# Performance work log

Measured on AMD Instinct MI355X. Metric: run time of the kernel, lower is better.

Reference implementation:

```python
import jax, jax.numpy as jnp
import numpy as np

B, D, H, DH = 2048, 1024, 8, 64  # batch, query_dim, heads, dim_head
INNER = H * DH  # 512


def setup_inputs() -> dict:
    key = jax.random.key(0)
    k0, k1, k2, k3 = jax.random.split(key, 4)
    x = jax.random.normal(k0, (B, D), dtype=jnp.float32)
    Wq = jax.random.normal(k1, (D, INNER), dtype=jnp.float32) * 0.02
    Wkv = jax.random.normal(k2, (D, 2 * INNER), dtype=jnp.float32) * 0.02
    Wout = jax.random.normal(k3, (INNER, D), dtype=jnp.float32) * 0.02
    bout = jnp.zeros((D,), dtype=jnp.float32)
    return {"x": x, "Wq": Wq, "Wkv": Wkv, "Wout": Wout, "bout": bout}


def reference(x, Wq, Wkv, Wout, bout):
    # Faithful to the original: 2D x, attention over the flattened (B*H) axis.
    b = x.shape[0]
    scale = DH ** -0.5
    q = (x @ Wq).reshape(b * H, DH)            # (b h) d
    k, v = jnp.split(x @ Wkv, 2, axis=-1)      # each [b, inner]
    k = k.reshape(b * H, DH)
    v = v.reshape(b * H, DH)
    sim = (q @ k.T) * scale                    # [(b h), (b h)] -- 1 GB intermediate
    attn = jax.nn.softmax(sim, axis=-1)        # dropout_rate = 0 -> identity
    out = (attn @ v).reshape(b, INNER)         # b (h d)
    return out @ Wout + bout                   # project_out path
```

## Files before the change

### kernel.cpp

```cpp
#include <hip/hip_runtime.h>
#include <hip/hip_bf16.h>
#include <stdint.h>


typedef __bf16 bf16_t;
typedef __bf16 bf16x4 __attribute__((ext_vector_type(4)));
typedef __bf16 bf16x8 __attribute__((ext_vector_type(8)));
typedef float floatx4 __attribute__((ext_vector_type(4)));

__device__ __forceinline__ floatx4 mfma16(bf16x8 a, bf16x8 b, floatx4 c) {
    return __builtin_amdgcn_mfma_f32_16x16x32_bf16(a, b, c, 0, 0, 0);
}

__device__ __forceinline__ bf16x8 cvt8(float4 a, float4 b) {
    bf16x8 o;
    o[0] = (bf16_t)a.x; o[1] = (bf16_t)a.y; o[2] = (bf16_t)a.z; o[3] = (bf16_t)a.w;
    o[4] = (bf16_t)b.x; o[5] = (bf16_t)b.y; o[6] = (bf16_t)b.z; o[7] = (bf16_t)b.w;
    return o;
}

__device__ __forceinline__ void transpose_body(const float* __restrict__ in, int N,
                                               bf16_t* __restrict__ out, int ldo,
                                               int bx, int by, int tid, float (*tile)[33]) {
    int n0 = bx * 32, k0 = by * 32;
    int tx = tid & 31, ty = tid >> 5;
#pragma unroll
    for (int i = 0; i < 32; i += 8)
        tile[ty + i][tx] = in[(size_t)(k0 + ty + i) * N + (n0 + tx)];
    __syncthreads();
#pragma unroll
    for (int i = 0; i < 32; i += 8)
        out[(size_t)(n0 + ty + i) * ldo + (k0 + tx)] = (bf16_t)tile[tx][ty + i];
}

__global__ __launch_bounds__(256) void prep_all(const float* __restrict__ x,
                                                bf16_t* __restrict__ xb,
                                                const float* __restrict__ Wq,
                                                const float* __restrict__ Wkv,
                                                const float* __restrict__ Wout,
                                                bf16_t* __restrict__ WtQKV,
                                                bf16_t* __restrict__ WtOut) {
    __shared__ float tile[32][33];
    int b = blockIdx.x, tid = threadIdx.x;
    if (b < 1024) {
        int i = (b * 256 + tid) * 8;
        *(bf16x8*)(xb + i) = cvt8(*(const float4*)(x + i), *(const float4*)(x + i + 4));
    } else if (b < 1536) {
        b -= 1024;
        transpose_body(Wq, 512, WtQKV, 1024, b & 15, b >> 4, tid, tile);
    } else if (b < 2560) {
        b -= 1536;
        transpose_body(Wkv, 1024, WtQKV + 512 * 1024, 1024, b & 31, b >> 5, tid, tile);
    } else {
        b -= 2560;
        transpose_body(Wout, 1024, WtOut, 512, b & 31, b >> 5, tid, tile);
    }
}

template <int OF32, int MI>
__global__ __launch_bounds__(256) void gemm_bt(const bf16_t* __restrict__ A,
                                               const bf16_t* __restrict__ Bt,
                                               const float* __restrict__ bias,
                                               void* __restrict__ Cout,
                                               bf16_t* __restrict__ VtOut, int vt_col0,
                                               int K, int lda, int ldb, int ldc,
                                               float qscale, int qcols) {
    constexpr int MT = MI * 32;
    constexpr int PA = MT / 64;
    __shared__ bf16_t sA[MT * 64];
    __shared__ bf16_t sB[64 * 64];
    int tid = threadIdx.x;
    int wave = tid >> 6, lane = tid & 63;
    int lm = lane & 15, q = lane >> 4;
    int bm = blockIdx.x * MT, bn = blockIdx.y * 64;
    int wm = (wave >> 1) * (MT / 2), wn = (wave & 1) * 32;

    int c0 = (tid & 3) * 2, c1 = c0 + 1;
    int rA[PA], swA[PA];
    size_t srcA0[PA], srcA1[PA];
#pragma unroll
    for (int p = 0; p < PA; ++p) {
        rA[p] = p * 64 + (tid >> 2);
        swA[p] = rA[p] & 7;
        srcA0[p] = (size_t)(bm + rA[p]) * lda + ((c0 ^ swA[p]) << 3);
        srcA1[p] = (size_t)(bm + rA[p]) * lda + ((c1 ^ swA[p]) << 3);
    }
    int rB = tid >> 2, swB = rB & 7;
    size_t srcB0 = (size_t)(bn + rB) * ldb + ((c0 ^ swB) << 3);
    size_t srcB1 = (size_t)(bn + rB) * ldb + ((c1 ^ swB) << 3);

    floatx4 acc[MI][2];
#pragma unroll
    for (int i = 0; i < MI; ++i)
#pragma unroll
        for (int j = 0; j < 2; ++j) acc[i][j] = (floatx4){0.f, 0.f, 0.f, 0.f};

    bf16x8 pa0[PA], pa1[PA], pb0, pb1;
#pragma unroll
    for (int p = 0; p < PA; ++p) {
        pa0[p] = *(const bf16x8*)(A + srcA0[p]);
        pa1[p] = *(const bf16x8*)(A + srcA1[p]);
    }
    pb0 = *(const bf16x8*)(Bt + srcB0);
    pb1 = *(const bf16x8*)(Bt + srcB1);
#pragma unroll
    for (int p = 0; p < PA; ++p) {
        *(bf16x8*)&sA[p * 4096 + tid * 16] = pa0[p];
        *(bf16x8*)&sA[p * 4096 + tid * 16 + 8] = pa1[p];
    }
    *(bf16x8*)&sB[tid * 16] = pb0;
    *(bf16x8*)&sB[tid * 16 + 8] = pb1;
    __syncthreads();

    for (int k0 = 0; k0 < K; k0 += 64) {
        int kn = (k0 + 64 < K) ? k0 + 64 : 0;
#pragma unroll
        for (int p = 0; p < PA; ++p) {
            pa0[p] = *(const bf16x8*)(A + srcA0[p] + kn);
            pa1[p] = *(const bf16x8*)(A + srcA1[p] + kn);
        }
        pb0 = *(const bf16x8*)(Bt + srcB0 + kn);
        pb1 = *(const bf16x8*)(Bt + srcB1 + kn);

#pragma unroll
        for (int s = 0; s < 2; ++s) {
            int cs = s * 4 + q;
            bf16x8 af[MI], bfr[2];
#pragma unroll
            for (int i = 0; i < MI; ++i) {
                int row = wm + i * 16 + lm;
                af[i] = *(bf16x8*)&sA[row * 64 + ((cs ^ (lm & 7)) << 3)];
            }
#pragma unroll
            for (int j = 0; j < 2; ++j) {
                int row = wn + j * 16 + lm;
                bfr[j] = *(bf16x8*)&sB[row * 64 + ((cs ^ (lm & 7)) << 3)];
            }
#pragma unroll
            for (int i = 0; i < MI; ++i)
#pragma unroll
                for (int j = 0; j < 2; ++j)
                    acc[i][j] = mfma16(af[i], bfr[j], acc[i][j]);
        }

        __syncthreads();
#pragma unroll
        for (int p = 0; p < PA; ++p) {
            *(bf16x8*)&sA[p * 4096 + tid * 16] = pa0[p];
            *(bf16x8*)&sA[p * 4096 + tid * 16 + 8] = pa1[p];
        }
        *(bf16x8*)&sB[tid * 16] = pb0;
        *(bf16x8*)&sB[tid * 16 + 8] = pb1;
        __syncthreads();
    }

#pragma unroll
    for (int i = 0; i < MI; ++i)
#pragma unroll
        for (int j = 0; j < 2; ++j)
#pragma unroll
            for (int r = 0; r < 4; ++r) {
                int row = bm + wm + i * 16 + q * 4 + r;
                int col = bn + wn + j * 16 + lm;
                float v = acc[i][j][r];
                if (col < qcols) v *= qscale;
                if (bias) v += bias[col];
                if (col >= vt_col0) {
                    int cc = col - vt_col0;
                    VtOut[(size_t)(cc & 63) * 16384 + row * 8 + (cc >> 6)] = (bf16_t)v;
                } else {
                    size_t off = (size_t)row * ldc + col;
                    if (OF32) ((float*)Cout)[off] = v;
                    else      ((bf16_t*)Cout)[off] = (bf16_t)v;
                }
            }
}

__global__ __launch_bounds__(256, 2) void flash_attn(const bf16_t* __restrict__ QK,
                                                     const bf16_t* __restrict__ Vt,
                                                     bf16_t* __restrict__ O,
                                                     float* __restrict__ accP,
                                                     float* __restrict__ lP,
                                                     int kps, int nsplit) {
    __shared__ bf16_t sK[2][64 * 64];
    __shared__ bf16_t sVt[2][64 * 64];
    int tid = threadIdx.x;
    int wave = tid >> 6, lane = tid & 63;
    int lm = lane & 15, q = lane >> 4;
    int sp = blockIdx.y;
    int qrow0 = blockIdx.x * 256 + wave * 64;

    bf16x8 qf[4][2];
#pragma unroll
    for (int sub = 0; sub < 4; ++sub) {
        int qr = qrow0 + sub * 16 + lm;
        const bf16_t* qp = QK + (size_t)(qr >> 3) * 1024 + (qr & 7) * 64;
        qf[sub][0] = *(const bf16x8*)(qp + q * 8);
        qf[sub][1] = *(const bf16x8*)(qp + 32 + q * 8);
    }

    int sr = tid >> 2;
    int ch0 = (tid & 3) * 2, ch1 = ch0 + 1;
    int swz = sr & 7;
    int lsr = 32 * (sr >> 5) + 8 * ((sr >> 2) & 3) + 4 * ((sr >> 4) & 1) + (sr & 3);
    int ksrcA = (lsr >> 3) * 1024 + (lsr & 7) * 64 + 512 + ((ch0 ^ swz) << 3);
    int ksrcB = (lsr >> 3) * 1024 + (lsr & 7) * 64 + 512 + ((ch1 ^ swz) << 3);
    size_t vsrcA = (size_t)sr * 16384 + ((ch0 ^ swz) << 3);
    size_t vsrcB = (size_t)sr * 16384 + ((ch1 ^ swz) << 3);

    int c0 = q ^ (lm & 7);

    floatx4 acc[4][4];
#pragma unroll
    for (int sub = 0; sub < 4; ++sub)
#pragma unroll
        for (int i = 0; i < 4; ++i) acc[sub][i] = (floatx4){0.f, 0.f, 0.f, 0.f};
    float lacc[4] = {0.f, 0.f, 0.f, 0.f};

    int kt0 = sp * kps, kend = kt0 + kps;

    bf16x8 krA, krB, vrA, vrB;
    {
        const bf16_t* kb = QK + (size_t)kt0 * 128;
        krA = *(const bf16x8*)(kb + ksrcA);
        krB = *(const bf16x8*)(kb + ksrcB);
        vrA = *(const bf16x8*)(Vt + vsrcA + kt0);
        vrB = *(const bf16x8*)(Vt + vsrcB + kt0);
    }
    *(bf16x8*)&sK[0][tid * 16] = krA; *(bf16x8*)&sK[0][tid * 16 + 8] = krB;
    *(bf16x8*)&sVt[0][tid * 16] = vrA; *(bf16x8*)&sVt[0][tid * 16 + 8] = vrB;
    __syncthreads();

    int cur = 0;
    for (int kt = kt0; kt < kend; kt += 64) {
        int ktn = (kt + 64 < kend) ? kt + 64 : kt0;
        const bf16_t* kbn = QK + (size_t)ktn * 128;
        krA = *(const bf16x8*)(kbn + ksrcA);
        krB = *(const bf16x8*)(kbn + ksrcB);
        vrA = *(const bf16x8*)(Vt + vsrcA + ktn);
        vrB = *(const bf16x8*)(Vt + vsrcB + ktn);

        const bf16_t* cK = sK[cur];
        const bf16_t* cV = sVt[cur];

        floatx4 s[4][4];
        __builtin_amdgcn_s_setprio(1);
#pragma unroll
        for (int nb = 0; nb < 4; ++nb) {
            int row = (nb * 16 + lm) * 64;
            bf16x8 k0 = *(const bf16x8*)&cK[row + (c0 << 3)];
            bf16x8 k1 = *(const bf16x8*)&cK[row + ((c0 ^ 4) << 3)];
#pragma unroll
            for (int sub = 0; sub < 4; ++sub) {
                floatx4 a = (floatx4){0.f, 0.f, 0.f, 0.f};
                a = mfma16(k0, qf[sub][0], a);
                a = mfma16(k1, qf[sub][1], a);
                s[sub][nb] = a;
            }
        }
        __builtin_amdgcn_s_setprio(0);

        bf16x8 pf[4][2];
#pragma unroll
        for (int sub = 0; sub < 4; ++sub) {
#pragma unroll
            for (int nb = 0; nb < 4; ++nb)
#pragma unroll
                for (int r = 0; r < 4; ++r) {
                    float pv = __builtin_amdgcn_exp2f(s[sub][nb][r]);
                    s[sub][nb][r] = pv;
                    lacc[sub] += pv;
                }
#pragma unroll
            for (int jb = 0; jb < 2; ++jb) {
                bf16x8 p;
#pragma unroll
                for (int r = 0; r < 4; ++r) {
                    p[r] = (bf16_t)s[sub][2 * jb][r];
                    p[r + 4] = (bf16_t)s[sub][2 * jb + 1][r];
                }
                pf[sub][jb] = p;
            }
        }

        __builtin_amdgcn_s_setprio(1);
#pragma unroll
        for (int jb = 0; jb < 2; ++jb) {
            bf16x8 av[4];
#pragma unroll
            for (int nd = 0; nd < 4; ++nd)
                av[nd] = *(const bf16x8*)&cV[(nd * 16 + lm) * 64 + ((c0 ^ (jb << 2)) << 3)];
#pragma unroll
            for (int sub = 0; sub < 4; ++sub)
#pragma unroll
                for (int nd = 0; nd < 4; ++nd)
                    acc[sub][nd] = mfma16(av[nd], pf[sub][jb], acc[sub][nd]);
        }
        __builtin_amdgcn_s_setprio(0);

        bf16_t* nK = &sK[cur ^ 1][tid * 16];
        bf16_t* nV = &sVt[cur ^ 1][tid * 16];
        *(bf16x8*)nK = krA; *(bf16x8*)(nK + 8) = krB;
        *(bf16x8*)nV = vrA; *(bf16x8*)(nV + 8) = vrB;
        __syncthreads();
        cur ^= 1;
    }

#pragma unroll
    for (int sub = 0; sub < 4; ++sub) {
        lacc[sub] += __shfl_xor(lacc[sub], 16);
        lacc[sub] += __shfl_xor(lacc[sub], 32);
    }

    if (nsplit == 1) {
#pragma unroll
        for (int sub = 0; sub < 4; ++sub) {
            float inv = 1.f / lacc[sub];
            int row = qrow0 + sub * 16 + lm;
#pragma unroll
            for (int nd = 0; nd < 4; ++nd) {
                bf16x4 o;
#pragma unroll
                for (int r = 0; r < 4; ++r) o[r] = (bf16_t)(acc[sub][nd][r] * inv);
                *(bf16x4*)&O[(size_t)row * 64 + nd * 16 + q * 4] = o;
            }
        }
    } else {
#pragma unroll
        for (int sub = 0; sub < 4; ++sub) {
            int row = qrow0 + sub * 16 + lm;
            size_t base = ((size_t)sp * 16384 + row) * 64;
#pragma unroll
            for (int nd = 0; nd < 4; ++nd) {
                float4 v = {acc[sub][nd][0], acc[sub][nd][1],
                            acc[sub][nd][2], acc[sub][nd][3]};
                *(float4*)&accP[base + nd * 16 + q * 4] = v;
            }
            if (lane < 16) lP[sp * 16384 + row] = lacc[sub];
        }
    }
}

__global__ __launch_bounds__(256) void merge_attn(const float* __restrict__ accP,
                                                  const float* __restrict__ lP,
                                                  bf16_t* __restrict__ O, int nsplit) {
    int idx = blockIdx.x * 256 + threadIdx.x;
    int row = idx >> 4, dh4 = (idx & 15) * 4;
    float4 num = {0.f, 0.f, 0.f, 0.f};
    float den = 0.f;
    for (int s = 0; s < nsplit; ++s) {
        float4 a = *(const float4*)&accP[((size_t)s * 16384 + row) * 64 + dh4];
        num.x += a.x; num.y += a.y; num.z += a.z; num.w += a.w;
        den += lP[s * 16384 + row];
    }
    float inv = 1.f / den;
    bf16x4 o;
    o[0] = (bf16_t)(num.x * inv); o[1] = (bf16_t)(num.y * inv);
    o[2] = (bf16_t)(num.z * inv); o[3] = (bf16_t)(num.w * inv);
    *(bf16x4*)&O[(size_t)row * 64 + dh4] = o;
}

extern "C" void kernel_launch(void* const* d_in, const int* in_sizes, int n_in,
                              void* d_out, int out_size, void* d_ws, size_t ws_size,
                              hipStream_t stream) {
    const float* x    = (const float*)d_in[0];
    const float* Wq   = (const float*)d_in[1];
    const float* Wkv  = (const float*)d_in[2];
    const float* Wout = (const float*)d_in[3];
    const float* bout = (const float*)d_in[4];

    char* ws = (char*)d_ws;
    bf16_t* QK    = (bf16_t*)ws;
    bf16_t* Vt    = (bf16_t*)(ws + 4194304);
    bf16_t* Ob    = (bf16_t*)(ws + 6291456);
    bf16_t* xb    = (bf16_t*)(ws + 8388608);
    bf16_t* WtQKV = (bf16_t*)(ws + 12582912);
    bf16_t* WtOut = (bf16_t*)(ws + 15728640);
    float*  accP  = (float*)(ws + 16777216);

    int nsplit = (ws_size >= (size_t)16777216 + 8 * 4259840) ? 8
               : (ws_size >= (size_t)16777216 + 4 * 4259840) ? 4
               : (ws_size >= (size_t)16777216 + 2 * 4259840) ? 2 : 1;
    float* lP = (float*)(ws + 16777216 + (size_t)nsplit * 4194304);

    prep_all<<<3072, 256, 0, stream>>>(x, xb, Wq, Wkv, Wout, WtQKV, WtOut);

    gemm_bt<0, 2><<<dim3(32, 24), 256, 0, stream>>>(
        xb, WtQKV, nullptr, QK, Vt, 1024, 1024, 1024, 1024, 1024,
        0.18033688011112042f, 512);

    flash_attn<<<dim3(64, nsplit), 256, 0, stream>>>(QK, Vt, Ob, accP, lP,
                                                     16384 / nsplit, nsplit);
    if (nsplit > 1)
        merge_attn<<<1024, 256, 0, stream>>>(accP, lP, Ob, nsplit);

    gemm_bt<1, 2><<<dim3(32, 16), 256, 0, stream>>>(
        Ob, WtOut, bout, d_out, nullptr, 1 << 30, 512, 512, 512, 1024,
        1.0f, 0);
}
```

Before: 172.4 us.

## Software-pipeline QK, softmax and PV across query sub-tiles in attention loop

Restructures the inner attention loop so the QK MFMAs for one query sub-tile are interleaved with the exp/convert and PV MFMAs of the previous sub-tile, using two ping-pong score buffers instead of a full 4x4 score array. The aim is to overlap transcendental VALU work with matrix-core work and to lower register pressure. It also removes the s_setprio hints and re-reads the V fragments from LDS for each sub-tile, which adds LDS traffic.

```diff
diff --git a/kernel.cpp b/kernel.cpp
--- a/kernel.cpp
+++ b/kernel.cpp
@@ -231,6 +231,41 @@
     *(bf16x8*)&sVt[0][tid * 16] = vrA; *(bf16x8*)&sVt[0][tid * 16 + 8] = vrB;
     __syncthreads();
 
+#define QK_SUB(S, sub)                                          \
+    _Pragma("unroll")                                           \
+    for (int nb = 0; nb < 4; ++nb) {                            \
+        floatx4 a_ = (floatx4){0.f, 0.f, 0.f, 0.f};             \
+        a_ = mfma16(kf0[nb], qf[sub][0], a_);                   \
+        a_ = mfma16(kf1[nb], qf[sub][1], a_);                   \
+        S[nb] = a_;                                             \
+    }
+
+#define SMPV_SUB(S, sub)                                                  \
+    {                                                                     \
+        _Pragma("unroll")                                                 \
+        for (int nb = 0; nb < 4; ++nb)                                    \
+            _Pragma("unroll")                                             \
+            for (int r = 0; r < 4; ++r) {                                 \
+                float pv_ = __builtin_amdgcn_exp2f(S[nb][r]);             \
+                S[nb][r] = pv_;                                           \
+                lacc[sub] += pv_;                                         \
+            }                                                             \
+        bf16x8 p0_, p1_;                                                  \
+        _Pragma("unroll")                                                 \
+        for (int r = 0; r < 4; ++r) {                                     \
+            p0_[r] = (bf16_t)S[0][r]; p0_[r + 4] = (bf16_t)S[1][r];       \
+            p1_[r] = (bf16_t)S[2][r]; p1_[r + 4] = (bf16_t)S[3][r];       \
+        }                                                                 \
+        _Pragma("unroll")                                                 \
+        for (int nd = 0; nd < 4; ++nd) {                                  \
+            int row_ = (nd * 16 + lm) * 64;                               \
+            bf16x8 v0_ = *(const bf16x8*)&cV[row_ + (c0 << 3)];           \
+            bf16x8 v1_ = *(const bf16x8*)&cV[row_ + ((c0 ^ 4) << 3)];     \
+            acc[sub][nd] = mfma16(v0_, p0_, acc[sub][nd]);                \
+            acc[sub][nd] = mfma16(v1_, p1_, acc[sub][nd]);                \
+        }                                                                 \
+    }
+
     int cur = 0;
     for (int kt = kt0; kt < kend; kt += 64) {
         int ktn = (kt + 64 < kend) ? kt + 64 : kt0;
@@ -243,60 +278,23 @@
         const bf16_t* cK = sK[cur];
         const bf16_t* cV = sVt[cur];
 
-        floatx4 s[4][4];
-        __builtin_amdgcn_s_setprio(1);
+        bf16x8 kf0[4], kf1[4];
 #pragma unroll
         for (int nb = 0; nb < 4; ++nb) {
             int row = (nb * 16 + lm) * 64;
-            bf16x8 k0 = *(const bf16x8*)&cK[row + (c0 << 3)];
-            bf16x8 k1 = *(const bf16x8*)&cK[row + ((c0 ^ 4) << 3)];
-#pragma unroll
-            for (int sub = 0; sub < 4; ++sub) {
-                floatx4 a = (floatx4){0.f, 0.f, 0.f, 0.f};
-                a = mfma16(k0, qf[sub][0], a);
-                a = mfma16(k1, qf[sub][1], a);
-                s[sub][nb] = a;
-            }
-        }
-        __builtin_amdgcn_s_setprio(0);
-
-        bf16x8 pf[4][2];
-#pragma unroll
-        for (int sub = 0; sub < 4; ++sub) {
-#pragma unroll
-            for (int nb = 0; nb < 4; ++nb)
-#pragma unroll
-                for (int r = 0; r < 4; ++r) {
-                    float pv = __builtin_amdgcn_exp2f(s[sub][nb][r]);
-                    s[sub][nb][r] = pv;
-                    lacc[sub] += pv;
-                }
-#pragma unroll
-            for (int jb = 0; jb < 2; ++jb) {
-                bf16x8 p;
-#pragma unroll
-                for (int r = 0; r < 4; ++r) {
-                    p[r] = (bf16_t)s[sub][2 * jb][r];
-                    p[r + 4] = (bf16_t)s[sub][2 * jb + 1][r];
-                }
-                pf[sub][jb] = p;
-            }
-        }
-
-        __builtin_amdgcn_s_setprio(1);
-#pragma unroll
-        for (int jb = 0; jb < 2; ++jb) {
-            bf16x8 av[4];
-#pragma unroll
-            for (int nd = 0; nd < 4; ++nd)
-                av[nd] = *(const bf16x8*)&cV[(nd * 16 + lm) * 64 + ((c0 ^ (jb << 2)) << 3)];
-#pragma unroll
-            for (int sub = 0; sub < 4; ++sub)
-#pragma unroll
-                for (int nd = 0; nd < 4; ++nd)
-                    acc[sub][nd] = mfma16(av[nd], pf[sub][jb], acc[sub][nd]);
-        }
-        __builtin_amdgcn_s_setprio(0);
+            kf0[nb] = *(const bf16x8*)&cK[row + (c0 << 3)];
+            kf1[nb] = *(const bf16x8*)&cK[row + ((c0 ^ 4) << 3)];
+        }
+
+        floatx4 sEv[4], sOd[4];
+        QK_SUB(sEv, 0);
+        QK_SUB(sOd, 1);
+        SMPV_SUB(sEv, 0);
+        QK_SUB(sEv, 2);
+        SMPV_SUB(sOd, 1);
+        QK_SUB(sOd, 3);
+        SMPV_SUB(sEv, 2);
+        SMPV_SUB(sOd, 3);
 
         bf16_t* nK = &sK[cur ^ 1][tid * 16];
         bf16_t* nV = &sVt[cur ^ 1][tid * 16];
@@ -305,6 +303,8 @@
         __syncthreads();
         cur ^= 1;
     }
+#undef QK_SUB
+#undef SMPV_SUB
 
 #pragma unroll
     for (int sub = 0; sub < 4; ++sub) {
```

After: 169.9 us (median of 2 runs). About the same (-1.4%).

## Switch flash attention to 32x32x16 MFMA tiles with interleaved QK/softmax/PV schedule

Applied to the files above, without the earlier changes.

Rewrites the attention inner loop to use 32x32x16 bf16 MFMA instructions instead of 16x16x32, which changes the Q/K/V fragment layouts, the K-row permutation used at load time, and the output write mapping. The QK^T, exp and PV stages are interleaved across two 32-key halves and two query sub-tiles so softmax ALU work can overlap with matrix instructions. Larger MFMA tiles cut LDS fragment reads per FLOP, but they raise accumulator register pressure. The explicit setprio hints are also removed.

```diff
diff --git a/kernel.cpp b/kernel.cpp
--- a/kernel.cpp
+++ b/kernel.cpp
@@ -7,9 +7,16 @@
 typedef __bf16 bf16x4 __attribute__((ext_vector_type(4)));
 typedef __bf16 bf16x8 __attribute__((ext_vector_type(8)));
 typedef float floatx4 __attribute__((ext_vector_type(4)));
+typedef float floatx16 __attribute__((ext_vector_type(16)));
+
+#define F16_ZERO (floatx16){0.f,0.f,0.f,0.f,0.f,0.f,0.f,0.f,0.f,0.f,0.f,0.f,0.f,0.f,0.f,0.f}
 
 __device__ __forceinline__ floatx4 mfma16(bf16x8 a, bf16x8 b, floatx4 c) {
     return __builtin_amdgcn_mfma_f32_16x16x32_bf16(a, b, c, 0, 0, 0);
+}
+
+__device__ __forceinline__ floatx16 mfma32(bf16x8 a, bf16x8 b, floatx16 c) {
+    return __builtin_amdgcn_mfma_f32_32x32x16_bf16(a, b, c, 0, 0, 0);
 }
 
 __device__ __forceinline__ bf16x8 cvt8(float4 a, float4 b) {
@@ -186,36 +193,38 @@
     __shared__ bf16_t sVt[2][64 * 64];
     int tid = threadIdx.x;
     int wave = tid >> 6, lane = tid & 63;
-    int lm = lane & 15, q = lane >> 4;
+    int lr = lane & 31, l5 = lane >> 5;
     int sp = blockIdx.y;
     int qrow0 = blockIdx.x * 256 + wave * 64;
 
-    bf16x8 qf[4][2];
-#pragma unroll
-    for (int sub = 0; sub < 4; ++sub) {
-        int qr = qrow0 + sub * 16 + lm;
-        const bf16_t* qp = QK + (size_t)(qr >> 3) * 1024 + (qr & 7) * 64;
-        qf[sub][0] = *(const bf16x8*)(qp + q * 8);
-        qf[sub][1] = *(const bf16x8*)(qp + 32 + q * 8);
+    bf16x8 qf[2][4];
+#pragma unroll
+    for (int sq = 0; sq < 2; ++sq) {
+        int qr = qrow0 + sq * 32 + lr;
+        const bf16_t* qp = QK + (size_t)(qr >> 3) * 1024 + (qr & 7) * 64 + l5 * 8;
+#pragma unroll
+        for (int c = 0; c < 4; ++c)
+            qf[sq][c] = *(const bf16x8*)(qp + c * 16);
     }
 
     int sr = tid >> 2;
     int ch0 = (tid & 3) * 2, ch1 = ch0 + 1;
     int swz = sr & 7;
-    int lsr = 32 * (sr >> 5) + 8 * ((sr >> 2) & 3) + 4 * ((sr >> 4) & 1) + (sr & 3);
+    int p_ = sr & 31;
+    int b4 = (p_ >> 2) & 3;
+    int sig = (b4 == 1 || b4 == 2) ? (p_ ^ 12) : p_;
+    int lsr = (sr & 32) + sig;
     int ksrcA = (lsr >> 3) * 1024 + (lsr & 7) * 64 + 512 + ((ch0 ^ swz) << 3);
     int ksrcB = (lsr >> 3) * 1024 + (lsr & 7) * 64 + 512 + ((ch1 ^ swz) << 3);
     size_t vsrcA = (size_t)sr * 16384 + ((ch0 ^ swz) << 3);
     size_t vsrcB = (size_t)sr * 16384 + ((ch1 ^ swz) << 3);
 
-    int c0 = q ^ (lm & 7);
-
-    floatx4 acc[4][4];
-#pragma unroll
-    for (int sub = 0; sub < 4; ++sub)
-#pragma unroll
-        for (int i = 0; i < 4; ++i) acc[sub][i] = (floatx4){0.f, 0.f, 0.f, 0.f};
-    float lacc[4] = {0.f, 0.f, 0.f, 0.f};
+    floatx16 acc[2][2];
+#pragma unroll
+    for (int sq = 0; sq < 2; ++sq)
+#pragma unroll
+        for (int i = 0; i < 2; ++i) acc[sq][i] = F16_ZERO;
+    float lacc[2] = {0.f, 0.f};
 
     int kt0 = sp * kps, kend = kt0 + kps;
 
@@ -230,6 +239,39 @@
     *(bf16x8*)&sK[0][tid * 16] = krA; *(bf16x8*)&sK[0][tid * 16 + 8] = krB;
     *(bf16x8*)&sVt[0][tid * 16] = vrA; *(bf16x8*)&sVt[0][tid * 16 + 8] = vrB;
     __syncthreads();
+
+#define QK_U(S, ts, sq)                                        \
+    {                                                          \
+        floatx16 a_ = F16_ZERO;                                \
+        _Pragma("unroll")                                      \
+        for (int c = 0; c < 4; ++c)                            \
+            a_ = mfma32(kf[ts][c], qf[sq][c], a_);             \
+        S = a_;                                                \
+    }
+
+#define SMPV_U(S, ts, sq)                                                            \
+    {                                                                                \
+        _Pragma("unroll")                                                            \
+        for (int r = 0; r < 16; ++r) {                                               \
+            float pv_ = __builtin_amdgcn_exp2f(S[r]);                                \
+            S[r] = pv_;                                                              \
+            lacc[sq] += pv_;                                                         \
+        }                                                                            \
+        bf16x8 pf0_, pf1_;                                                           \
+        _Pragma("unroll")                                                            \
+        for (int r = 0; r < 8; ++r) {                                                \
+            pf0_[r] = (bf16_t)S[r];                                                  \
+            pf1_[r] = (bf16_t)S[r + 8];                                              \
+        }                                                                            \
+        _Pragma("unroll")                                                            \
+        for (int nd2 = 0; nd2 < 2; ++nd2) {                                          \
+            int row_ = (nd2 * 32 + lr) * 64;                                         \
+            bf16x8 v0_ = *(const bf16x8*)&cV[row_ + ((((ts)*4 + l5) ^ (lr & 7)) << 3)];     \
+            bf16x8 v1_ = *(const bf16x8*)&cV[row_ + ((((ts)*4 + 2 + l5) ^ (lr & 7)) << 3)]; \
+            acc[sq][nd2] = mfma32(v0_, pf0_, acc[sq][nd2]);                          \
+            acc[sq][nd2] = mfma32(v1_, pf1_, acc[sq][nd2]);                          \
+        }                                                                            \
+    }
 
     int cur = 0;
     for (int kt = kt0; kt < kend; kt += 64) {
@@ -243,60 +285,23 @@
         const bf16_t* cK = sK[cur];
         const bf16_t* cV = sVt[cur];
 
-        floatx4 s[4][4];
-        __builtin_amdgcn_s_setprio(1);
-#pragma unroll
-        for (int nb = 0; nb < 4; ++nb) {
-            int row = (nb * 16 + lm) * 64;
-            bf16x8 k0 = *(const bf16x8*)&cK[row + (c0 << 3)];
-            bf16x8 k1 = *(const bf16x8*)&cK[row + ((c0 ^ 4) << 3)];
-#pragma unroll
-            for (int sub = 0; sub < 4; ++sub) {
-                floatx4 a = (floatx4){0.f, 0.f, 0.f, 0.f};
-                a = mfma16(k0, qf[sub][0], a);
-                a = mfma16(k1, qf[sub][1], a);
-                s[sub][nb] = a;
-            }
-        }
-        __builtin_amdgcn_s_setprio(0);
-
-        bf16x8 pf[4][2];
-#pragma unroll
-        for (int sub = 0; sub < 4; ++sub) {
-#pragma unroll
-            for (int nb = 0; nb < 4; ++nb)
-#pragma unroll
-                for (int r = 0; r < 4; ++r) {
-                    float pv = __builtin_amdgcn_exp2f(s[sub][nb][r]);
-                    s[sub][nb][r] = pv;
-                    lacc[sub] += pv;
-                }
-#pragma unroll
-            for (int jb = 0; jb < 2; ++jb) {
-                bf16x8 p;
-#pragma unroll
-                for (int r = 0; r < 4; ++r) {
-                    p[r] = (bf16_t)s[sub][2 * jb][r];
-                    p[r + 4] = (bf16_t)s[sub][2 * jb + 1][r];
-                }
-                pf[sub][jb] = p;
-            }
-        }
-
-        __builtin_amdgcn_s_setprio(1);
-#pragma unroll
-        for (int jb = 0; jb < 2; ++jb) {
-            bf16x8 av[4];
-#pragma unroll
-            for (int nd = 0; nd < 4; ++nd)
-                av[nd] = *(const bf16x8*)&cV[(nd * 16 + lm) * 64 + ((c0 ^ (jb << 2)) << 3)];
-#pragma unroll
-            for (int sub = 0; sub < 4; ++sub)
-#pragma unroll
-                for (int nd = 0; nd < 4; ++nd)
-                    acc[sub][nd] = mfma16(av[nd], pf[sub][jb], acc[sub][nd]);
-        }
-        __builtin_amdgcn_s_setprio(0);
+        bf16x8 kf[2][4];
+#pragma unroll
+        for (int ts = 0; ts < 2; ++ts)
+#pragma unroll
+            for (int c = 0; c < 4; ++c)
+                kf[ts][c] = *(const bf16x8*)
+                    &cK[(ts * 32 + lr) * 64 + (((2 * c + l5) ^ (lr & 7)) << 3)];
+
+        floatx16 sA_, sB_;
+        QK_U(sA_, 0, 0);
+        QK_U(sB_, 0, 1);
+        SMPV_U(sA_, 0, 0);
+        QK_U(sA_, 1, 0);
+        SMPV_U(sB_, 0, 1);
+        QK_U(sB_, 1, 1);
+        SMPV_U(sA_, 1, 0);
+        SMPV_U(sB_, 1, 1);
 
         bf16_t* nK = &sK[cur ^ 1][tid * 16];
         bf16_t* nV = &sVt[cur ^ 1][tid * 16];
@@ -305,38 +310,44 @@
         __syncthreads();
         cur ^= 1;
     }
-
-#pragma unroll
-    for (int sub = 0; sub < 4; ++sub) {
-        lacc[sub] += __shfl_xor(lacc[sub], 16);
-        lacc[sub] += __shfl_xor(lacc[sub], 32);
-    }
+#undef QK_U
+#undef SMPV_U
+
+    lacc[0] += __shfl_xor(lacc[0], 32);
+    lacc[1] += __shfl_xor(lacc[1], 32);
 
     if (nsplit == 1) {
 #pragma unroll
-        for (int sub = 0; sub < 4; ++sub) {
-            float inv = 1.f / lacc[sub];
-            int row = qrow0 + sub * 16 + lm;
-#pragma unroll
-            for (int nd = 0; nd < 4; ++nd) {
-                bf16x4 o;
-#pragma unroll
-                for (int r = 0; r < 4; ++r) o[r] = (bf16_t)(acc[sub][nd][r] * inv);
-                *(bf16x4*)&O[(size_t)row * 64 + nd * 16 + q * 4] = o;
-            }
+        for (int sq = 0; sq < 2; ++sq) {
+            float inv = 1.f / lacc[sq];
+            int row = qrow0 + sq * 32 + lr;
+#pragma unroll
+            for (int nd2 = 0; nd2 < 2; ++nd2)
+#pragma unroll
+                for (int g = 0; g < 4; ++g) {
+                    bf16x4 o;
+#pragma unroll
+                    for (int r = 0; r < 4; ++r)
+                        o[r] = (bf16_t)(acc[sq][nd2][4 * g + r] * inv);
+                    int dh = nd2 * 32 + 8 * g + 4 * l5;
+                    *(bf16x4*)&O[(size_t)row * 64 + dh] = o;
+                }
         }
     } else {
 #pragma unroll
-        for (int sub = 0; sub < 4; ++sub) {
-            int row = qrow0 + sub * 16 + lm;
+        for (int sq = 0; sq < 2; ++sq) {
+            int row = qrow0 + sq * 32 + lr;
             size_t base = ((size_t)sp * 16384 + row) * 64;
 #pragma unroll
-            for (int nd = 0; nd < 4; ++nd) {
-                float4 v = {acc[sub][nd][0], acc[sub][nd][1],
-                            acc[sub][nd][2], acc[sub][nd][3]};
-                *(float4*)&accP[base + nd * 16 + q * 4] = v;
-            }
-            if (lane < 16) lP[sp * 16384 + row] = lacc[sub];
+            for (int nd2 = 0; nd2 < 2; ++nd2)
+#pragma unroll
+                for (int g = 0; g < 4; ++g) {
+                    float4 v = {acc[sq][nd2][4 * g], acc[sq][nd2][4 * g + 1],
+                                acc[sq][nd2][4 * g + 2], acc[sq][nd2][4 * g + 3]};
+                    int dh = nd2 * 32 + 8 * g + 4 * l5;
+                    *(float4*)&accP[base + dh] = v;
+                }
+            if (lane < 32) lP[sp * 16384 + row] = lacc[sq];
         }
     }
 }
```

Measured after the change: 176.9 us. 1.03x slower.
